# Optimization experiments

Hardware: AMD Instinct MI355X
Metric: run time of the kernel (lower is better)

## Reference

```python
import jax, jax.numpy as jnp
import numpy as np

N_USER = 100000
N_ITEM = 200000


def setup_inputs() -> dict:
    key = jax.random.key(0)
    ks = jax.random.split(key, 9)
    n = N_USER + N_ITEM
    nnz = 9600000
    return {
        "users_emb": jax.random.normal(ks[0], (N_USER, 64), dtype=jnp.float32) * 0.1,
        "items_emb": jax.random.normal(ks[1], (N_ITEM, 64), dtype=jnp.float32) * 0.1,
        "user_sim_neighbor": jax.random.randint(ks[2], (N_USER, 10), 0, N_USER),
        "user_sim_weight": jax.random.uniform(ks[3], (N_USER, 10), dtype=jnp.float32),
        "item_sim_neighbor": jax.random.randint(ks[4], (N_ITEM, 10), 0, N_ITEM),
        "item_sim_weight": jax.random.uniform(ks[5], (N_ITEM, 10), dtype=jnp.float32),
        "graph_rows": jax.random.randint(ks[6], (nnz,), 0, n),
        "graph_cols": jax.random.randint(ks[7], (nnz,), 0, n),
        "graph_vals": jax.random.uniform(ks[8], (nnz,), dtype=jnp.float32),
    }


def reference(users_emb, items_emb, user_sim_neighbor, user_sim_weight,
              item_sim_neighbor, item_sim_weight, graph_rows, graph_cols, graph_vals):
    n = users_emb.shape[0] + items_emb.shape[0]
    emb = jnp.concatenate([users_emb, items_emb], axis=0)  # [n, d]

    # top-k neighbor gather + weighted sum (users then items)
    user_neighbor_emb = jnp.einsum("nk,nkd->nd", user_sim_weight, users_emb[user_sim_neighbor])
    item_neighbor_emb = jnp.einsum("nk,nkd->nd", item_sim_weight, items_emb[item_sim_neighbor])
    neighbor_emb = jnp.concatenate([user_neighbor_emb, item_neighbor_emb], axis=0)

    # sparse graph matmul: all_emb = Graph @ emb  (COO rows/cols/vals)
    all_emb = jax.ops.segment_sum(graph_vals[:, None] * emb[graph_cols], graph_rows,
                                  num_segments=n)

    emb = emb + neighbor_emb + all_emb
    users = emb[:users_emb.shape[0]]
    items = emb[users_emb.shape[0]:]
    return users, items
```

## Files before the change

kernel.cpp:

```cpp
#include <hip/hip_runtime.h>

#define N_USER 100000
#define N_ITEM 200000
#define N_TOT  (N_USER + N_ITEM)
#define D      64
#define RPB    64
#define NB     ((N_TOT + RPB - 1) / RPB)
#define NBLK_A 256
#define THR_A  512
#define CAP    2304
#define SCAN_CHUNK 2048

__device__ __forceinline__ unsigned short f2bf(float f) {
    unsigned b = __float_as_uint(f);
    unsigned r = (b + 0x7FFFu + ((b >> 16) & 1u)) >> 16;
    return (unsigned short)r;
}
__device__ __forceinline__ float bf2f(unsigned short u) {
    return __uint_as_float(((unsigned)u) << 16);
}

__global__ __launch_bounds__(256) void conv_kernel(const float* __restrict__ users,
                                                   const float* __restrict__ items,
                                                   ushort* __restrict__ emb16) {
    size_t i = (size_t)blockIdx.x * blockDim.x + threadIdx.x;
    const size_t total = (size_t)N_TOT * D / 4;
    if (i >= total) return;
    size_t e0 = i * 4;
    const size_t usz = (size_t)N_USER * D;
    const float* src = (e0 < usz) ? users + e0 : items + (e0 - usz);
    float4 v = *reinterpret_cast<const float4*>(src);
    ushort4 o;
    o.x = f2bf(v.x); o.y = f2bf(v.y); o.z = f2bf(v.z); o.w = f2bf(v.w);
    *reinterpret_cast<ushort4*>(emb16 + e0) = o;
}


__global__ __launch_bounds__(THR_A) void hist_kernel(const int* __restrict__ rows,
                                                     int* __restrict__ hist, int nnz, int chunk) {
    __shared__ int h[NB];
    for (int k = threadIdx.x; k < NB; k += blockDim.x) h[k] = 0;
    __syncthreads();
    int lo = blockIdx.x * chunk;
    int hi = min(lo + chunk, nnz);
    for (int i = lo + threadIdx.x; i < hi; i += blockDim.x)
        atomicAdd(&h[rows[i] >> 6], 1);
    __syncthreads();
    for (int k = threadIdx.x; k < NB; k += blockDim.x)
        hist[(size_t)blockIdx.x * NB + k] = h[k];
}

__global__ void bucket_tot_kernel(const int* __restrict__ hist, int* __restrict__ tot) {
    int k = blockIdx.x * blockDim.x + threadIdx.x;
    if (k >= NB) return;
    int s = 0;
    for (int b = 0; b < NBLK_A; ++b) s += hist[(size_t)b * NB + k];
    tot[k] = s;
}

__global__ __launch_bounds__(1024) void scan_kernel(const int* __restrict__ tot,
                                                    int* __restrict__ bstart, int nnz) {
    __shared__ int s[1024];
    const int t = threadIdx.x;
    const int PER = (NB + 1023) / 1024;
    int loc[8];
    int sum = 0;
    #pragma unroll
    for (int k = 0; k < PER; ++k) {
        int idx = t * PER + k;
        int v = (idx < NB) ? tot[idx] : 0;
        loc[k] = sum; sum += v;
    }
    s[t] = sum;
    __syncthreads();
    for (int off = 1; off < 1024; off <<= 1) {
        int v = (t >= off) ? s[t - off] : 0;
        __syncthreads();
        s[t] += v;
        __syncthreads();
    }
    int base = s[t] - sum;
    #pragma unroll
    for (int k = 0; k < PER; ++k) {
        int idx = t * PER + k;
        if (idx < NB) bstart[idx] = base + loc[k];
    }
    if (t == 1023) bstart[NB] = nnz;
}

__global__ void blockbase_kernel(int* __restrict__ hist, const int* __restrict__ bstart) {
    int k = blockIdx.x * blockDim.x + threadIdx.x;
    if (k >= NB) return;
    int base = bstart[k];
    for (int b = 0; b < NBLK_A; ++b) {
        size_t idx = (size_t)b * NB + k;
        int v = hist[idx];
        hist[idx] = base;
        base += v;
    }
}

__global__ __launch_bounds__(THR_A) void bin_kernel(const int* __restrict__ rows,
                                                    const int* __restrict__ cols,
                                                    const float* __restrict__ vals,
                                                    const int* __restrict__ hist,
                                                    uint2* __restrict__ eg, int nnz, int chunk) {
    __shared__ int cur[NB];
    for (int k = threadIdx.x; k < NB; k += blockDim.x)
        cur[k] = hist[(size_t)blockIdx.x * NB + k];
    __syncthreads();
    int lo = blockIdx.x * chunk;
    int hi = min(lo + chunk, nnz);
    for (int i = lo + threadIdx.x; i < hi; i += blockDim.x) {
        int r = rows[i];
        int k = r >> 6;
        int slot = atomicAdd(&cur[k], 1);
        uint2 p;
        p.x = ((unsigned)(r & 63) << 19) | (unsigned)cols[i];
        p.y = __float_as_uint(vals[i]);
        eg[slot] = p;
    }
}

__global__ __launch_bounds__(256) void sortgather_kernel(
    const float* __restrict__ users, const float* __restrict__ items,
    const ushort* __restrict__ emb16,
    const int*   __restrict__ unb,   const float* __restrict__ uw,
    const int*   __restrict__ inb,   const float* __restrict__ iw,
    const int*   __restrict__ bstart, const uint2* __restrict__ eg,
    float* __restrict__ out)
{
    __shared__ uint2 lds_e[CAP];
    __shared__ int h[RPB], st[RPB], cur[RPB];

    const int tid  = threadIdx.x;
    const int g    = tid >> 4;
    const int sub  = tid & 15;
    const int d0   = sub * 4;
    const int k    = blockIdx.x;
    const int row0 = k * RPB;

    float4 acc[4];
    #pragma unroll
    for (int rr = 0; rr < 4; ++rr) {
        const int row = row0 + rr * 16 + g;
        if (row >= N_TOT) { acc[rr] = make_float4(0.f, 0.f, 0.f, 0.f); continue; }
        float4 a;
        if (row < N_USER) {
            a = *reinterpret_cast<const float4*>(&users[(size_t)row * D + d0]);
            const int*   nb = unb + (size_t)row * 10;
            const float* w  = uw  + (size_t)row * 10;
            #pragma unroll
            for (int q = 0; q < 10; ++q) {
                ushort4 u = *reinterpret_cast<const ushort4*>(emb16 + (size_t)nb[q] * D + d0);
                float wq = w[q];
                a.x += wq * bf2f(u.x); a.y += wq * bf2f(u.y);
                a.z += wq * bf2f(u.z); a.w += wq * bf2f(u.w);
            }
        } else {
            const int r = row - N_USER;
            a = *reinterpret_cast<const float4*>(&items[(size_t)r * D + d0]);
            const int*   nb = inb + (size_t)r * 10;
            const float* w  = iw  + (size_t)r * 10;
            #pragma unroll
            for (int q = 0; q < 10; ++q) {
                ushort4 u = *reinterpret_cast<const ushort4*>(emb16 + ((size_t)nb[q] + N_USER) * D + d0);
                float wq = w[q];
                a.x += wq * bf2f(u.x); a.y += wq * bf2f(u.y);
                a.z += wq * bf2f(u.z); a.w += wq * bf2f(u.w);
            }
        }
        acc[rr] = a;
    }

    const int s = bstart[k];
    const int e = bstart[k + 1];

    for (int cs = s; cs < e; cs += CAP) {
        const int n = min(e - cs, CAP);

        if (tid < RPB) h[tid] = 0;
        __syncthreads();
        for (int i = tid; i < n; i += 256)
            atomicAdd(&h[eg[cs + i].x >> 19], 1);
        __syncthreads();
        if (tid < RPB) {
            int orig = h[tid];
            int v = orig;
            #pragma unroll
            for (int off = 1; off < RPB; off <<= 1) {
                int u = __shfl_up(v, off);
                if (tid >= off) v += u;
            }
            st[tid]  = v - orig;
            cur[tid] = v - orig;
        }
        __syncthreads();
        for (int i = tid; i < n; i += 256) {
            uint2 p = eg[cs + i];
            int slot = atomicAdd(&cur[p.x >> 19], 1);
            lds_e[slot] = p;
        }
        __syncthreads();

        #pragma unroll
        for (int rr = 0; rr < 4; ++rr) {
            const int r  = rr * 16 + g;
            const int b0 = st[r];
            const int cr = h[r];
            int j = 0;
            for (; j + 3 < cr; j += 4) {
                uint2 p0 = lds_e[b0 + j],     p1 = lds_e[b0 + j + 1];
                uint2 p2 = lds_e[b0 + j + 2], p3 = lds_e[b0 + j + 3];
                ushort4 u0 = *reinterpret_cast<const ushort4*>(emb16 + (size_t)(p0.x & 0x7FFFFu) * D + d0);
                ushort4 u1 = *reinterpret_cast<const ushort4*>(emb16 + (size_t)(p1.x & 0x7FFFFu) * D + d0);
                ushort4 u2 = *reinterpret_cast<const ushort4*>(emb16 + (size_t)(p2.x & 0x7FFFFu) * D + d0);
                ushort4 u3 = *reinterpret_cast<const ushort4*>(emb16 + (size_t)(p3.x & 0x7FFFFu) * D + d0);
                float a0 = __uint_as_float(p0.y), a1 = __uint_as_float(p1.y);
                float a2 = __uint_as_float(p2.y), a3 = __uint_as_float(p3.y);
                acc[rr].x += a0 * bf2f(u0.x); acc[rr].y += a0 * bf2f(u0.y);
                acc[rr].z += a0 * bf2f(u0.z); acc[rr].w += a0 * bf2f(u0.w);
                acc[rr].x += a1 * bf2f(u1.x); acc[rr].y += a1 * bf2f(u1.y);
                acc[rr].z += a1 * bf2f(u1.z); acc[rr].w += a1 * bf2f(u1.w);
                acc[rr].x += a2 * bf2f(u2.x); acc[rr].y += a2 * bf2f(u2.y);
                acc[rr].z += a2 * bf2f(u2.z); acc[rr].w += a2 * bf2f(u2.w);
                acc[rr].x += a3 * bf2f(u3.x); acc[rr].y += a3 * bf2f(u3.y);
                acc[rr].z += a3 * bf2f(u3.z); acc[rr].w += a3 * bf2f(u3.w);
            }
            for (; j < cr; ++j) {
                uint2 p = lds_e[b0 + j];
                ushort4 u = *reinterpret_cast<const ushort4*>(emb16 + (size_t)(p.x & 0x7FFFFu) * D + d0);
                float a = __uint_as_float(p.y);
                acc[rr].x += a * bf2f(u.x); acc[rr].y += a * bf2f(u.y);
                acc[rr].z += a * bf2f(u.z); acc[rr].w += a * bf2f(u.w);
            }
        }
        __syncthreads();
    }

    #pragma unroll
    for (int rr = 0; rr < 4; ++rr) {
        const int row = row0 + rr * 16 + g;
        if (row < N_TOT)
            *reinterpret_cast<float4*>(&out[(size_t)row * D + d0]) = acc[rr];
    }
}


__global__ void count_kernel(const int* __restrict__ rows, int* __restrict__ cnt, int nnz) {
    int i = blockIdx.x * blockDim.x + threadIdx.x;
    int stride = gridDim.x * blockDim.x;
    for (; i < nnz; i += stride) atomicAdd(&cnt[rows[i]], 1);
}

__global__ void scan_block_sums(const int* __restrict__ cnt, int* __restrict__ bsum, int n) {
    __shared__ int sdata[256];
    int base = blockIdx.x * SCAN_CHUNK;
    int s = 0;
    for (int t = threadIdx.x; t < SCAN_CHUNK; t += 256) {
        int idx = base + t;
        s += (idx < n) ? cnt[idx] : 0;
    }
    sdata[threadIdx.x] = s;
    __syncthreads();
    for (int off = 128; off > 0; off >>= 1) {
        if (threadIdx.x < off) sdata[threadIdx.x] += sdata[threadIdx.x + off];
        __syncthreads();
    }
    if (threadIdx.x == 0) bsum[blockIdx.x] = sdata[0];
}

__global__ void scan_bsum_kernel(int* __restrict__ bsum, int nb) {
    if (threadIdx.x == 0 && blockIdx.x == 0) {
        int acc = 0;
        for (int i = 0; i < nb; ++i) { int v = bsum[i]; bsum[i] = acc; acc += v; }
    }
}

__global__ void scan_final(const int* __restrict__ cnt, const int* __restrict__ bsum,
                           int* __restrict__ row_start, int n, int nnz) {
    __shared__ int sums[256];
    int b = blockIdx.x, t = threadIdx.x;
    int base = b * SCAN_CHUNK;
    int loc[8];
    int s = 0;
    #pragma unroll
    for (int k = 0; k < 8; ++k) {
        int idx = base + t * 8 + k;
        int v = (idx < n) ? cnt[idx] : 0;
        loc[k] = s; s += v;
    }
    sums[t] = s;
    __syncthreads();
    for (int off = 1; off < 256; off <<= 1) {
        int v = (t >= off) ? sums[t - off] : 0;
        __syncthreads();
        sums[t] += v;
        __syncthreads();
    }
    int off0 = bsum[b] + (sums[t] - s);
    #pragma unroll
    for (int k = 0; k < 8; ++k) {
        int idx = base + t * 8 + k;
        if (idx < n) row_start[idx] = off0 + loc[k];
    }
    if (b == gridDim.x - 1 && t == 255) row_start[n] = nnz;
}

__global__ void fill_kernel(const int* __restrict__ rows, const int* __restrict__ cols,
                            const float* __restrict__ vals, const int* __restrict__ row_start,
                            int* __restrict__ pos, uint2* __restrict__ eg, int nnz) {
    int i = blockIdx.x * blockDim.x + threadIdx.x;
    int stride = gridDim.x * blockDim.x;
    for (; i < nnz; i += stride) {
        int r = rows[i];
        int p = atomicAdd(&pos[r], 1);
        uint2 e;
        e.x = (unsigned)cols[i];
        e.y = __float_as_uint(vals[i]);
        eg[row_start[r] + p] = e;
    }
}

__global__ __launch_bounds__(256) void gather16_kernel(
    const float* __restrict__ users, const float* __restrict__ items,
    const int*   __restrict__ unb,   const float* __restrict__ uw,
    const int*   __restrict__ inb,   const float* __restrict__ iw,
    const int*   __restrict__ row_start, const uint2* __restrict__ eg,
    float* __restrict__ out)
{
    const int tid = threadIdx.x;
    const int grp = tid >> 4;
    const int sub = tid & 15;
    const int row = blockIdx.x * 16 + grp;
    if (row >= N_TOT) return;
    const int d0 = sub * 4;

    float4 acc;
    if (row < N_USER) {
        acc = *reinterpret_cast<const float4*>(&users[(size_t)row * D + d0]);
        const int*   nb = unb + (size_t)row * 10;
        const float* w  = uw  + (size_t)row * 10;
        #pragma unroll
        for (int q = 0; q < 10; ++q) {
            float4 v = *reinterpret_cast<const float4*>(&users[(size_t)nb[q] * D + d0]);
            float wq = w[q];
            acc.x += wq * v.x; acc.y += wq * v.y; acc.z += wq * v.z; acc.w += wq * v.w;
        }
    } else {
        int r = row - N_USER;
        acc = *reinterpret_cast<const float4*>(&items[(size_t)r * D + d0]);
        const int*   nb = inb + (size_t)r * 10;
        const float* w  = iw  + (size_t)r * 10;
        #pragma unroll
        for (int q = 0; q < 10; ++q) {
            float4 v = *reinterpret_cast<const float4*>(&items[(size_t)nb[q] * D + d0]);
            float wq = w[q];
            acc.x += wq * v.x; acc.y += wq * v.y; acc.z += wq * v.z; acc.w += wq * v.w;
        }
    }

    const int s = row_start[row];
    const int e = row_start[row + 1];
    int i = s;
    for (; i + 3 < e; i += 4) {
        uint2 p0 = eg[i], p1 = eg[i + 1], p2 = eg[i + 2], p3 = eg[i + 3];
        int c0 = (int)(p0.x & 0x7FFFFu), c1 = (int)(p1.x & 0x7FFFFu);
        int c2 = (int)(p2.x & 0x7FFFFu), c3 = (int)(p3.x & 0x7FFFFu);
        const float* s0 = (c0 < N_USER) ? users + (size_t)c0 * D : items + (size_t)(c0 - N_USER) * D;
        const float* s1 = (c1 < N_USER) ? users + (size_t)c1 * D : items + (size_t)(c1 - N_USER) * D;
        const float* s2 = (c2 < N_USER) ? users + (size_t)c2 * D : items + (size_t)(c2 - N_USER) * D;
        const float* s3 = (c3 < N_USER) ? users + (size_t)c3 * D : items + (size_t)(c3 - N_USER) * D;
        float4 v0 = *reinterpret_cast<const float4*>(s0 + d0);
        float4 v1 = *reinterpret_cast<const float4*>(s1 + d0);
        float4 v2 = *reinterpret_cast<const float4*>(s2 + d0);
        float4 v3 = *reinterpret_cast<const float4*>(s3 + d0);
        float a0 = __uint_as_float(p0.y), a1 = __uint_as_float(p1.y);
        float a2 = __uint_as_float(p2.y), a3 = __uint_as_float(p3.y);
        acc.x += a0 * v0.x; acc.y += a0 * v0.y; acc.z += a0 * v0.z; acc.w += a0 * v0.w;
        acc.x += a1 * v1.x; acc.y += a1 * v1.y; acc.z += a1 * v1.z; acc.w += a1 * v1.w;
        acc.x += a2 * v2.x; acc.y += a2 * v2.y; acc.z += a2 * v2.z; acc.w += a2 * v2.w;
        acc.x += a3 * v3.x; acc.y += a3 * v3.y; acc.z += a3 * v3.z; acc.w += a3 * v3.w;
    }
    for (; i < e; ++i) {
        uint2 p = eg[i];
        int c = (int)(p.x & 0x7FFFFu);
        const float* src = (c < N_USER) ? users + (size_t)c * D : items + (size_t)(c - N_USER) * D;
        float4 v = *reinterpret_cast<const float4*>(src + d0);
        float a = __uint_as_float(p.y);
        acc.x += a * v.x; acc.y += a * v.y; acc.z += a * v.z; acc.w += a * v.w;
    }

    *reinterpret_cast<float4*>(&out[(size_t)row * D + d0]) = acc;
}

__global__ __launch_bounds__(256) void base_neighbor_kernel(
    const float* __restrict__ users, const float* __restrict__ items,
    const int*   __restrict__ unb,   const float* __restrict__ uw,
    const int*   __restrict__ inb,   const float* __restrict__ iw,
    float* __restrict__ out)
{
    int gtid = blockIdx.x * blockDim.x + threadIdx.x;
    int row  = gtid >> 6;
    int lane = gtid & 63;
    if (row >= N_TOT) return;
    float acc;
    if (row < N_USER) {
        acc = users[(size_t)row * D + lane];
        const int*   nb = unb + (size_t)row * 10;
        const float* w  = uw  + (size_t)row * 10;
        #pragma unroll
        for (int q = 0; q < 10; ++q) acc += w[q] * users[(size_t)nb[q] * D + lane];
    } else {
        int r = row - N_USER;
        acc = items[(size_t)r * D + lane];
        const int*   nb = inb + (size_t)r * 10;
        const float* w  = iw  + (size_t)r * 10;
        #pragma unroll
        for (int q = 0; q < 10; ++q) acc += w[q] * items[(size_t)nb[q] * D + lane];
    }
    out[(size_t)row * D + lane] = acc;
}

__global__ __launch_bounds__(256) void edge_scatter_kernel(
    const float* __restrict__ users, const float* __restrict__ items,
    const int*   __restrict__ rows,  const int* __restrict__ cols,
    const float* __restrict__ vals,
    float* __restrict__ out, int nnz)
{
    int gtid = blockIdx.x * blockDim.x + threadIdx.x;
    int e    = gtid >> 6;
    int lane = gtid & 63;
    if (e >= nnz) return;
    int   r = rows[e];
    int   c = cols[e];
    float v = vals[e];
    const float* src = (c < N_USER) ? (users + (size_t)c * D)
                                    : (items + (size_t)(c - N_USER) * D);
    atomicAdd(&out[(size_t)r * D + lane], v * src[lane]);
}

extern "C" void kernel_launch(void* const* d_in, const int* in_sizes, int n_in,
                              void* d_out, int out_size, void* d_ws, size_t ws_size,
                              hipStream_t stream) {
    const float* users = (const float*)d_in[0];
    const float* items = (const float*)d_in[1];
    const int*   unb   = (const int*)  d_in[2];
    const float* uw    = (const float*)d_in[3];
    const int*   inb   = (const int*)  d_in[4];
    const float* iw    = (const float*)d_in[5];
    const int*   grow  = (const int*)  d_in[6];
    const int*   gcol  = (const int*)  d_in[7];
    const float* gval  = (const float*)d_in[8];
    float* out = (float*)d_out;

    const int nnz = in_sizes[6];

    const size_t A = 255;
    const size_t sz_eg       = (((size_t)nnz * 8) + A) & ~A;
    const size_t sz_hist     = (((size_t)NBLK_A * NB * 4) + A) & ~A;
    const size_t sz_tot      = (((size_t)NB * 4) + A) & ~A;
    const size_t sz_bstart   = (((size_t)(NB + 1) * 4) + A) & ~A;
    const size_t sz_rowstart = (((size_t)(N_TOT + 1) * 4) + A) & ~A;
    const size_t sz_emb16    = (((size_t)N_TOT * D * 2) + A) & ~A;
    const size_t need0 = sz_eg + sz_hist + sz_tot + sz_bstart + sz_emb16;

    const size_t sz_cnt  = (((size_t)N_TOT * 4) + A) & ~A;
    const int    nb2     = (N_TOT + SCAN_CHUNK - 1) / SCAN_CHUNK;
    const size_t sz_bsum = (((size_t)nb2 * 4) + A) & ~A;
    const size_t need2 = sz_eg + sz_rowstart + sz_cnt + sz_bsum;

    if (ws_size >= need0) {
        char* wsp = (char*)d_ws;
        uint2*  eg        = (uint2*)wsp;  wsp += sz_eg;
        int*    hist      = (int*)wsp;    wsp += sz_hist;
        int*    tot       = (int*)wsp;    wsp += sz_tot;
        int*    bstart    = (int*)wsp;    wsp += sz_bstart;
        ushort* emb16     = (ushort*)wsp;

        const int chunk = (nnz + NBLK_A - 1) / NBLK_A;
        const int conv_grid = (int)(((size_t)N_TOT * D / 4 + 255) / 256);

        conv_kernel<<<conv_grid, 256, 0, stream>>>(users, items, emb16);
        hist_kernel<<<NBLK_A, THR_A, 0, stream>>>(grow, hist, nnz, chunk);
        bucket_tot_kernel<<<(NB + 255) / 256, 256, 0, stream>>>(hist, tot);
        scan_kernel<<<1, 1024, 0, stream>>>(tot, bstart, nnz);
        blockbase_kernel<<<(NB + 255) / 256, 256, 0, stream>>>(hist, bstart);
        bin_kernel<<<NBLK_A, THR_A, 0, stream>>>(grow, gcol, gval, hist, eg, nnz, chunk);
        sortgather_kernel<<<NB, 256, 0, stream>>>(users, items, emb16, unb, uw, inb, iw,
                                                  bstart, eg, out);
    } else if (ws_size >= need2) {
        char* wsp = (char*)d_ws;
        uint2* eg        = (uint2*)wsp;  wsp += sz_eg;
        int*   row_start = (int*)wsp;    wsp += sz_rowstart;
        int*   cnt       = (int*)wsp;    wsp += sz_cnt;
        int*   bsum      = (int*)wsp;

        hipMemsetAsync(cnt, 0, (size_t)N_TOT * 4, stream);
        count_kernel<<<2048, 256, 0, stream>>>(grow, cnt, nnz);
        scan_block_sums<<<nb2, 256, 0, stream>>>(cnt, bsum, N_TOT);
        scan_bsum_kernel<<<1, 64, 0, stream>>>(bsum, nb2);
        scan_final<<<nb2, 256, 0, stream>>>(cnt, bsum, row_start, N_TOT, nnz);
        hipMemsetAsync(cnt, 0, (size_t)N_TOT * 4, stream);
        fill_kernel<<<2048, 256, 0, stream>>>(grow, gcol, gval, row_start, cnt, eg, nnz);
        const int g16_grid = (N_TOT + 15) / 16;
        gather16_kernel<<<g16_grid, 256, 0, stream>>>(users, items, unb, uw, inb, iw,
                                                      row_start, eg, out);
    } else {
        int grid = (int)(((long long)N_TOT * 64 + 255) / 256);
        base_neighbor_kernel<<<grid, 256, 0, stream>>>(users, items, unb, uw, inb, iw, out);
        long long ethreads = (long long)nnz * 64;
        long long egrid = (ethreads + 255) / 256;
        edge_scatter_kernel<<<(int)egrid, 256, 0, stream>>>(users, items, grow, gcol, gval, out, nnz);
    }
}
```

Before: 562.0 us.

## Replace per-block histogram matrix with global atomic bucket offsets and fuse binning passes

Drops the per-block histogram matrix along with the bucket_tot and blockbase kernels. Each counting block now atomically adds its local bucket counts into a global total. The fill kernel recomputes its local histogram and reserves per-bucket slot ranges from a global cursor with atomics, with the block count raised from 256 to 512. The gather kernel also reads the self embedding from the bf16 copy instead of the fp32 inputs. This cuts kernel launches and the serial strided hist passes, but reads the row indices an extra time, makes intra-bucket order nondeterministic, and lowers precision of the self term.

After: 571.6 us. Within noise of the previous version (+1.7%).

```diff
diff --git a/kernel.cpp b/kernel.cpp
--- a/kernel.cpp
+++ b/kernel.cpp
@@ -6,7 +6,7 @@
 #define D      64
 #define RPB    64
 #define NB     ((N_TOT + RPB - 1) / RPB)
-#define NBLK_A 256
+#define NBLK_F 512
 #define THR_A  512
 #define CAP    2304
 #define SCAN_CHUNK 2048
@@ -36,8 +36,8 @@
 }
 
 
-__global__ __launch_bounds__(THR_A) void hist_kernel(const int* __restrict__ rows,
-                                                     int* __restrict__ hist, int nnz, int chunk) {
+__global__ __launch_bounds__(THR_A) void count_fused(const int* __restrict__ rows,
+                                                     int* __restrict__ tot, int nnz, int chunk) {
     __shared__ int h[NB];
     for (int k = threadIdx.x; k < NB; k += blockDim.x) h[k] = 0;
     __syncthreads();
@@ -47,19 +47,12 @@
         atomicAdd(&h[rows[i] >> 6], 1);
     __syncthreads();
     for (int k = threadIdx.x; k < NB; k += blockDim.x)
-        hist[(size_t)blockIdx.x * NB + k] = h[k];
-}
-
-__global__ void bucket_tot_kernel(const int* __restrict__ hist, int* __restrict__ tot) {
-    int k = blockIdx.x * blockDim.x + threadIdx.x;
-    if (k >= NB) return;
-    int s = 0;
-    for (int b = 0; b < NBLK_A; ++b) s += hist[(size_t)b * NB + k];
-    tot[k] = s;
+        if (h[k]) atomicAdd(&tot[k], h[k]);
 }
 
 __global__ __launch_bounds__(1024) void scan_kernel(const int* __restrict__ tot,
-                                                    int* __restrict__ bstart, int nnz) {
+                                                    int* __restrict__ bstart,
+                                                    int* __restrict__ gcur, int nnz) {
     __shared__ int s[1024];
     const int t = threadIdx.x;
     const int PER = (NB + 1023) / 1024;
@@ -83,38 +76,31 @@
     #pragma unroll
     for (int k = 0; k < PER; ++k) {
         int idx = t * PER + k;
-        if (idx < NB) bstart[idx] = base + loc[k];
+        if (idx < NB) { bstart[idx] = base + loc[k]; gcur[idx] = base + loc[k]; }
     }
     if (t == 1023) bstart[NB] = nnz;
 }
 
-__global__ void blockbase_kernel(int* __restrict__ hist, const int* __restrict__ bstart) {
-    int k = blockIdx.x * blockDim.x + threadIdx.x;
-    if (k >= NB) return;
-    int base = bstart[k];
-    for (int b = 0; b < NBLK_A; ++b) {
-        size_t idx = (size_t)b * NB + k;
-        int v = hist[idx];
-        hist[idx] = base;
-        base += v;
-    }
-}
-
-__global__ __launch_bounds__(THR_A) void bin_kernel(const int* __restrict__ rows,
+__global__ __launch_bounds__(THR_A) void fill_fused(const int* __restrict__ rows,
                                                     const int* __restrict__ cols,
                                                     const float* __restrict__ vals,
-                                                    const int* __restrict__ hist,
+                                                    int* __restrict__ gcur,
                                                     uint2* __restrict__ eg, int nnz, int chunk) {
-    __shared__ int cur[NB];
-    for (int k = threadIdx.x; k < NB; k += blockDim.x)
-        cur[k] = hist[(size_t)blockIdx.x * NB + k];
+    __shared__ int h[NB];
+    for (int k = threadIdx.x; k < NB; k += blockDim.x) h[k] = 0;
     __syncthreads();
     int lo = blockIdx.x * chunk;
     int hi = min(lo + chunk, nnz);
+    for (int i = lo + threadIdx.x; i < hi; i += blockDim.x)
+        atomicAdd(&h[rows[i] >> 6], 1);
+    __syncthreads();
+    for (int k = threadIdx.x; k < NB; k += blockDim.x)
+        if (h[k]) h[k] = atomicAdd(&gcur[k], h[k]);
+    __syncthreads();
     for (int i = lo + threadIdx.x; i < hi; i += blockDim.x) {
         int r = rows[i];
         int k = r >> 6;
-        int slot = atomicAdd(&cur[k], 1);
+        int slot = atomicAdd(&h[k], 1);
         uint2 p;
         p.x = ((unsigned)(r & 63) << 19) | (unsigned)cols[i];
         p.y = __float_as_uint(vals[i]);
@@ -123,7 +109,6 @@
 }
 
 __global__ __launch_bounds__(256) void sortgather_kernel(
-    const float* __restrict__ users, const float* __restrict__ items,
     const ushort* __restrict__ emb16,
     const int*   __restrict__ unb,   const float* __restrict__ uw,
     const int*   __restrict__ inb,   const float* __restrict__ iw,
@@ -145,9 +130,9 @@
     for (int rr = 0; rr < 4; ++rr) {
         const int row = row0 + rr * 16 + g;
         if (row >= N_TOT) { acc[rr] = make_float4(0.f, 0.f, 0.f, 0.f); continue; }
-        float4 a;
+        ushort4 ub = *reinterpret_cast<const ushort4*>(emb16 + (size_t)row * D + d0);
+        float4 a = make_float4(bf2f(ub.x), bf2f(ub.y), bf2f(ub.z), bf2f(ub.w));
         if (row < N_USER) {
-            a = *reinterpret_cast<const float4*>(&users[(size_t)row * D + d0]);
             const int*   nb = unb + (size_t)row * 10;
             const float* w  = uw  + (size_t)row * 10;
             #pragma unroll
@@ -159,7 +144,6 @@
             }
         } else {
             const int r = row - N_USER;
-            a = *reinterpret_cast<const float4*>(&items[(size_t)r * D + d0]);
             const int*   nb = inb + (size_t)r * 10;
             const float* w  = iw  + (size_t)r * 10;
             #pragma unroll
@@ -458,12 +442,12 @@
 
     const size_t A = 255;
     const size_t sz_eg       = (((size_t)nnz * 8) + A) & ~A;
-    const size_t sz_hist     = (((size_t)NBLK_A * NB * 4) + A) & ~A;
     const size_t sz_tot      = (((size_t)NB * 4) + A) & ~A;
     const size_t sz_bstart   = (((size_t)(NB + 1) * 4) + A) & ~A;
+    const size_t sz_gcur     = (((size_t)NB * 4) + A) & ~A;
     const size_t sz_rowstart = (((size_t)(N_TOT + 1) * 4) + A) & ~A;
     const size_t sz_emb16    = (((size_t)N_TOT * D * 2) + A) & ~A;
-    const size_t need0 = sz_eg + sz_hist + sz_tot + sz_bstart + sz_emb16;
+    const size_t need0 = sz_eg + sz_tot + sz_bstart + sz_gcur + sz_emb16;
 
     const size_t sz_cnt  = (((size_t)N_TOT * 4) + A) & ~A;
     const int    nb2     = (N_TOT + SCAN_CHUNK - 1) / SCAN_CHUNK;
@@ -472,22 +456,21 @@
 
     if (ws_size >= need0) {
         char* wsp = (char*)d_ws;
-        uint2*  eg        = (uint2*)wsp;  wsp += sz_eg;
-        int*    hist      = (int*)wsp;    wsp += sz_hist;
-        int*    tot       = (int*)wsp;    wsp += sz_tot;
-        int*    bstart    = (int*)wsp;    wsp += sz_bstart;
-        ushort* emb16     = (ushort*)wsp;
-
-        const int chunk = (nnz + NBLK_A - 1) / NBLK_A;
+        uint2*  eg     = (uint2*)wsp;  wsp += sz_eg;
+        int*    tot    = (int*)wsp;    wsp += sz_tot;
+        int*    bstart = (int*)wsp;    wsp += sz_bstart;
+        int*    gcur   = (int*)wsp;    wsp += sz_gcur;
+        ushort* emb16  = (ushort*)wsp;
+
+        const int chunk = (nnz + NBLK_F - 1) / NBLK_F;
         const int conv_grid = (int)(((size_t)N_TOT * D / 4 + 255) / 256);
 
         conv_kernel<<<conv_grid, 256, 0, stream>>>(users, items, emb16);
-        hist_kernel<<<NBLK_A, THR_A, 0, stream>>>(grow, hist, nnz, chunk);
-        bucket_tot_kernel<<<(NB + 255) / 256, 256, 0, stream>>>(hist, tot);
-        scan_kernel<<<1, 1024, 0, stream>>>(tot, bstart, nnz);
-        blockbase_kernel<<<(NB + 255) / 256, 256, 0, stream>>>(hist, bstart);
-        bin_kernel<<<NBLK_A, THR_A, 0, stream>>>(grow, gcol, gval, hist, eg, nnz, chunk);
-        sortgather_kernel<<<NB, 256, 0, stream>>>(users, items, emb16, unb, uw, inb, iw,
+        hipMemsetAsync(tot, 0, (size_t)NB * 4, stream);
+        count_fused<<<NBLK_F, THR_A, 0, stream>>>(grow, tot, nnz, chunk);
+        scan_kernel<<<1, 1024, 0, stream>>>(tot, bstart, gcur, nnz);
+        fill_fused<<<NBLK_F, THR_A, 0, stream>>>(grow, gcol, gval, gcur, eg, nnz, chunk);
+        sortgather_kernel<<<NB, 256, 0, stream>>>(emb16, unb, uw, inb, iw,
                                                   bstart, eg, out);
     } else if (ws_size >= need2) {
         char* wsp = (char*)d_ws;
```
